# Kernel optimization log

Hardware: AMD Instinct MI355X
Metric: run time of the kernel (lower is better)

## Reference

```python
import jax, jax.numpy as jnp
import numpy as np

B, S, F_ATT, R, A = 1024, 96, 2048, 512, 512  # batch, att_size, att_feat_size, rnn_size, att_hid_size

def setup_inputs() -> dict:
    key = jax.random.key(0)
    ks = jax.random.split(key, 16)
    def lin(k, out_d, in_d):
        s = 1.0 / np.sqrt(in_d)
        kw, kb = jax.random.split(k)
        return (jax.random.uniform(kw, (out_d, in_d), jnp.float32, -s, s),
                jax.random.uniform(kb, (out_d,), jnp.float32, -s, s))
    W_ae, b_ae = lin(ks[0], R, F_ATT)   # att_embed Linear
    W_c,  b_c  = lin(ks[1], A, R)       # ctx2att
    W_s,  b_s  = lin(ks[2], A, R)       # sentinel_embed
    W_h,  b_h  = lin(ks[3], A, R)       # ho_embed
    W_al, b_al = lin(ks[4], 1, A)       # alpha_net
    W_o,  b_o  = lin(ks[5], R, R)       # att2h
    return {
        'h': jax.random.normal(ks[6], (B, R), jnp.float32),
        'sentinel': jax.random.normal(ks[7], (B, R), jnp.float32),
        'att_feats': jax.random.normal(ks[8], (B, S, F_ATT), jnp.float32),
        'W_ae': W_ae, 'b_ae': b_ae, 'W_c': W_c, 'b_c': b_c,
        'W_s': W_s, 'b_s': b_s, 'W_h': W_h, 'b_h': b_h,
        'W_al': W_al, 'b_al': b_al, 'W_o': W_o, 'b_o': b_o,
    }

def reference(h, sentinel, att_feats, W_ae, b_ae, W_c, b_c, W_s, b_s,
              W_h, b_h, W_al, b_al, W_o, b_o):
    # att_embed: Linear(2048->512) + ReLU (dropout = identity in eval)
    att = jax.nn.relu(jnp.einsum('bsf,rf->bsr', att_feats, W_ae) + b_ae)  # [B,S,R]
    att_embd = jnp.einsum('bsr,ar->bsa', att, W_c) + b_c                   # [B,S,A]
    sent_e = sentinel @ W_s.T + b_s                                        # [B,A]
    h_e = h @ W_h.T + b_h                                                  # [B,A]
    # concat sentinel slot in front of attention features
    img_all = jnp.concatenate([sentinel[:, None, :], att], axis=1)         # [B,S+1,R]
    img_all_embed = jnp.concatenate([sent_e[:, None, :], att_embd], axis=1)  # [B,S+1,A]
    hA = jnp.tanh(img_all_embed + h_e[:, None, :])                         # [B,S+1,A]
    logits = jnp.einsum('bsa,a->bs', hA, W_al[0]) + b_al[0]                # [B,S+1]
    alpha = jax.nn.softmax(logits, axis=-1)
    cHat = jnp.einsum('bs,bsr->br', alpha, img_all)                        # [B,R]
    atten_out = cHat + h
    return jnp.tanh(atten_out @ W_o.T + b_o)                               # [B,R]
```

## Files before the change

### kernel.cpp

```cpp
#include <hip/hip_runtime.h>

#define M1 98304
#define RDIM 512
#define FDIM 2048
#define SDIM 96
#define BM 96
#define BK 64

typedef __attribute__((ext_vector_type(8))) __bf16 bf16x8;
typedef __attribute__((ext_vector_type(4))) float f32x4;
typedef __attribute__((ext_vector_type(2))) float f32x2;

#define WAITV6 asm volatile("s_waitcnt vmcnt(6)" ::: "memory")
#define WAITV3 asm volatile("s_waitcnt vmcnt(3)" ::: "memory")
#define WAITV0 asm volatile("s_waitcnt vmcnt(0)" ::: "memory")
#define WAITL0 asm volatile("s_waitcnt lgkmcnt(0)" ::: "memory")
#define SBAR   __builtin_amdgcn_s_barrier()
#define SCHED0 __builtin_amdgcn_sched_barrier(0)

__device__ __forceinline__ float bf2f(unsigned short u){
  union { unsigned int i; float f; } v; v.i = ((unsigned int)u) << 16; return v.f;
}
__device__ __forceinline__ unsigned short f2bf(float f){
  union { float f; unsigned int i; } v; v.f = f;
  unsigned int r = v.i + 0x7FFFu + ((v.i >> 16) & 1u);
  return (unsigned short)(r >> 16);
}
__device__ __forceinline__ unsigned short f2bfn(float f){
  __bf16 b = (__bf16)f;
  return __builtin_bit_cast(unsigned short, b);
}
__device__ __forceinline__ float fast_tanh(float x){
  float e = __expf(2.f * x);
  return 1.f - 2.f / (e + 1.f);
}
__device__ __forceinline__ void gld_lds16(const void* g, void* l){
  __builtin_amdgcn_global_load_lds((const __attribute__((address_space(1))) void*)g,
                                   (__attribute__((address_space(3))) void*)l, 16, 0, 0);
}
__device__ __forceinline__ f32x4 mfma16(bf16x8 a, bf16x8 b, f32x4 c){
  return __builtin_amdgcn_mfma_f32_16x16x32_bf16(a, b, c, 0, 0, 0);
}
__device__ __forceinline__ f32x2 ntload2(const float* p){
  return __builtin_nontemporal_load(reinterpret_cast<const f32x2*>(p));
}

__device__ __forceinline__ void cat_store_a(const float* __restrict__ src,
                                            unsigned short* __restrict__ dst, int idx){
  float x = src[idx];
  int r = idx >> 9, c = idx & 511;
  unsigned short hi = f2bf(x);
  unsigned short lo = f2bf(x - bf2f(hi));
  unsigned short* p = dst + (long)r * 1536 + c;
  p[0] = hi; p[512] = lo; p[1024] = hi;
}
__device__ __forceinline__ void cat_store_w(const float* __restrict__ src,
                                            unsigned short* __restrict__ dst, int idx){
  float x = src[idx];
  int r = idx >> 9, c = idx & 511;
  unsigned short hi = f2bf(x);
  unsigned short lo = f2bf(x - bf2f(hi));
  unsigned short* p = dst + (long)r * 1536 + c;
  p[0] = hi; p[512] = hi; p[1024] = lo;
}

__global__ void k_convert(const float* W_ae, const float* W_c, const float* W_s,
                          const float* W_h, const float* W_o,
                          const float* h, const float* sent,
                          unsigned short* W_ae_bf, unsigned short* W_c_bf,
                          unsigned short* W_s_cat, unsigned short* W_h_cat,
                          unsigned short* W_o_cat, unsigned short* h_cat,
                          unsigned short* s_cat){
  const int stride = 1024 * 256;
  int i0 = blockIdx.x * 256 + threadIdx.x;
  switch (blockIdx.y) {
    case 0: for (int i = i0; i < 512*2048; i += stride) W_ae_bf[i] = f2bf(W_ae[i]); break;
    case 1: for (int i = i0; i < 512*512;  i += stride) W_c_bf[i]  = f2bf(W_c[i]);  break;
    case 2: for (int i = i0; i < 512*512;  i += stride) cat_store_w(W_s, W_s_cat, i); break;
    case 3: for (int i = i0; i < 512*512;  i += stride) cat_store_w(W_h, W_h_cat, i); break;
    case 4: for (int i = i0; i < 512*512;  i += stride) cat_store_w(W_o, W_o_cat, i); break;
    case 5: for (int i = i0; i < 1024*512; i += stride) cat_store_a(h, h_cat, i); break;
    case 6: for (int i = i0; i < 1024*512; i += stride) cat_store_a(sent, s_cat, i); break;
  }
}

__global__ __launch_bounds__(1024, 4) void k_fused(
    const float* __restrict__ Af, const unsigned short* __restrict__ Wae,
    const float* __restrict__ b_ae,
    const unsigned short* __restrict__ Wcg, const float* __restrict__ b_c,
    const float* __restrict__ h_e, const float* __restrict__ W_al,
    const float* __restrict__ sent_e, const float* __restrict__ sent,
    const float* __restrict__ hvec, unsigned short* __restrict__ atten_cat){
  __shared__ __align__(16) char smem[155648];
  unsigned short* As   = (unsigned short*)smem;
  unsigned short* Bs   = (unsigned short*)(smem + 24576);
  unsigned short* attL = (unsigned short*)smem;
  unsigned short* Wcs  = (unsigned short*)(smem + 98304);
  float* part = (float*)(smem + 131072);
  float* lg   = (float*)(smem + 131072 + 3072);
  float* alp  = (float*)(smem + 131072 + 3072 + 512);
  float* ssum = (float*)(smem + 131072 + 3072 + 1024);

  const int tid = threadIdx.x;
  const int w = tid >> 6, l = tid & 63;
  const int wm = w >> 3, wn = w & 7;
  const int b = blockIdx.x;
  const long m0 = (long)b * BM;
  const int g = l >> 4, r15 = l & 15;
  const int rs = r15 & 7;

  f32x4 acc[3][4];
#pragma unroll
  for (int i = 0; i < 3; ++i)
#pragma unroll
    for (int j = 0; j < 4; ++j) acc[i][j] = f32x4{0.f,0.f,0.f,0.f};

  {
    const int bswz = (l & 7) ^ (l >> 3);
    const unsigned short* bbase = Wae + (long)(w*32 + (l >> 3)) * FDIM + bswz*8;
    int aswz[3];
    const float* abase[3];
#pragma unroll
    for (int s = 0; s < 3; ++s) {
      int c = tid + s*1024;
      int row = c >> 5, kp = c & 31;
      abase[s] = Af + (m0 + row)*FDIM + kp*2;
      aswz[s] = row*BK + (((kp>>1) ^ ((row&7)<<1))<<2) + ((kp&1)<<1);
    }
    const int NT = FDIM / BK;
    f32x2 d0,d1,d2, e0,e1,e2;
    f32x2 f0 = {0,0}, f1 = {0,0}, f2 = {0,0};

    {
      f32x2 c0 = ntload2(abase[0]);
      f32x2 c1 = ntload2(abase[1]);
      f32x2 c2 = ntload2(abase[2]);
      SCHED0;
#pragma unroll
      for (int q = 0; q < 4; ++q)
        gld_lds16(bbase + (long)q*8*FDIM, Bs + w*2048 + q*512);
      SCHED0;
      d0 = ntload2(abase[0] + BK);
      d1 = ntload2(abase[1] + BK);
      d2 = ntload2(abase[2] + BK);
      e0 = ntload2(abase[0] + 2*BK);
      e1 = ntload2(abase[1] + 2*BK);
      e2 = ntload2(abase[2] + 2*BK);
      SCHED0;
      *reinterpret_cast<unsigned int*>(&As[aswz[0]]) =
          (unsigned int)f2bfn(c0.x) | ((unsigned int)f2bfn(c0.y) << 16);
      *reinterpret_cast<unsigned int*>(&As[aswz[1]]) =
          (unsigned int)f2bfn(c1.x) | ((unsigned int)f2bfn(c1.y) << 16);
      *reinterpret_cast<unsigned int*>(&As[aswz[2]]) =
          (unsigned int)f2bfn(c2.x) | ((unsigned int)f2bfn(c2.y) << 16);
      WAITV6; WAITL0; SCHED0; SBAR; SCHED0;
    }

    int cb = 0;
    for (int kt = 0; kt < NT; ++kt) {
      const int nb = cb ^ 1;
      if (kt + 1 < NT) {
        const long kof = (long)(kt+1) * BK;
#pragma unroll
        for (int q = 0; q < 4; ++q)
          gld_lds16(bbase + (long)q*8*FDIM + kof, Bs + nb*32768 + w*2048 + q*512);
      }
      SCHED0;
      if (kt + 3 < NT) {
        const long kof = (long)(kt+3) * BK;
        f0 = ntload2(abase[0] + kof);
        f1 = ntload2(abase[1] + kof);
        f2 = ntload2(abase[2] + kof);
      }
      SCHED0;
#pragma unroll
      for (int hh = 0; hh < 2; ++hh) {
        const int ko = ((g + 4*hh) ^ rs) << 3;
        bf16x8 afr[3], bfr[4];
#pragma unroll
        for (int i = 0; i < 3; ++i)
          afr[i] = *reinterpret_cast<const bf16x8*>(&As[cb*6144 + (wm*48 + i*16 + r15)*BK + ko]);
#pragma unroll
        for (int j = 0; j < 4; ++j)
          bfr[j] = *reinterpret_cast<const bf16x8*>(&Bs[cb*32768 + (wn*64 + j*16 + r15)*BK + ko]);
        __builtin_amdgcn_s_setprio(1);
#pragma unroll
        for (int i = 0; i < 3; ++i)
#pragma unroll
          for (int j = 0; j < 4; ++j)
            acc[i][j] = mfma16(afr[i], bfr[j], acc[i][j]);
        __builtin_amdgcn_s_setprio(0);
      }
      if (kt + 1 < NT) {
        *reinterpret_cast<unsigned int*>(&As[nb*6144 + aswz[0]]) =
            (unsigned int)f2bfn(d0.x) | ((unsigned int)f2bfn(d0.y) << 16);
        *reinterpret_cast<unsigned int*>(&As[nb*6144 + aswz[1]]) =
            (unsigned int)f2bfn(d1.x) | ((unsigned int)f2bfn(d1.y) << 16);
        *reinterpret_cast<unsigned int*>(&As[nb*6144 + aswz[2]]) =
            (unsigned int)f2bfn(d2.x) | ((unsigned int)f2bfn(d2.y) << 16);
        d0=e0; d1=e1; d2=e2; e0=f0; e1=f1; e2=f2;
        if (kt + 3 < NT) { WAITV3; } else { WAITV0; }
        WAITL0; SCHED0; SBAR; SCHED0;
        cb = nb;
      }
    }
  }
  __syncthreads();
  {
    float bb[4];
#pragma unroll
    for (int j = 0; j < 4; ++j) bb[j] = b_ae[wn*64 + j*16 + r15];
#pragma unroll
    for (int i = 0; i < 3; ++i)
#pragma unroll
      for (int r = 0; r < 4; ++r) {
        int row = wm*48 + i*16 + g*4 + r;
        int rs8 = row & 7;
#pragma unroll
        for (int j = 0; j < 4; ++j) {
          int col = wn*64 + j*16 + r15;
          float x = acc[i][j][r] + bb[j];
          x = x > 0.f ? x : 0.f;
          attL[row*512 + (((col>>3) ^ rs8)<<3) + (col&7)] = f2bfn(x);
        }
      }
  }
  __syncthreads();

#pragma unroll
  for (int i = 0; i < 3; ++i)
#pragma unroll
    for (int j = 0; j < 4; ++j) acc[i][j] = f32x4{0.f,0.f,0.f,0.f};
  {
    const int lr = l >> 2;
    const int bsl2 = (l & 3) ^ ((l >> 3) & 3);
    const int rs2 = (r15 >> 1) & 3;
    uint4 rr0, rr1;
    rr0 = *reinterpret_cast<const uint4*>(Wcg + (long)(w*32 + 0*16 + lr)*RDIM + bsl2*8);
    rr1 = *reinterpret_cast<const uint4*>(Wcg + (long)(w*32 + 1*16 + lr)*RDIM + bsl2*8);
    for (int kt = 0; kt < 16; ++kt) {
      *reinterpret_cast<uint4*>(&Wcs[w*1024 + 0*512 + l*8]) = rr0;
      *reinterpret_cast<uint4*>(&Wcs[w*1024 + 1*512 + l*8]) = rr1;
      if (kt < 15) {
        const int k0 = (kt+1)*32;
        rr0 = *reinterpret_cast<const uint4*>(Wcg + (long)(w*32 + 0*16 + lr)*RDIM + k0 + bsl2*8);
        rr1 = *reinterpret_cast<const uint4*>(Wcg + (long)(w*32 + 1*16 + lr)*RDIM + k0 + bsl2*8);
      }
      WAITL0; SCHED0; SBAR; SCHED0;
      bf16x8 afr[3], bfr[4];
#pragma unroll
      for (int i = 0; i < 3; ++i) {
        int ra = wm*48 + i*16 + r15;
        int grp = (kt<<2) + g;
        afr[i] = *reinterpret_cast<const bf16x8*>(&attL[ra*512 + ((grp ^ rs)<<3)]);
      }
#pragma unroll
      for (int j = 0; j < 4; ++j)
        bfr[j] = *reinterpret_cast<const bf16x8*>(&Wcs[(wn*64 + j*16 + r15)*32 + ((g ^ rs2)<<3)]);
      __builtin_amdgcn_s_setprio(1);
#pragma unroll
      for (int i = 0; i < 3; ++i)
#pragma unroll
        for (int j = 0; j < 4; ++j)
          acc[i][j] = mfma16(afr[i], bfr[j], acc[i][j]);
      __builtin_amdgcn_s_setprio(0);
      WAITL0; SCHED0; SBAR; SCHED0;
    }
  }
  {
    const float* hrow = h_e + (long)b * RDIM;
    float bb2[4], wa[4], he[4];
#pragma unroll
    for (int j = 0; j < 4; ++j) {
      int n = wn*64 + j*16 + r15;
      bb2[j] = b_c[n]; wa[j] = W_al[n]; he[j] = hrow[n];
    }
#pragma unroll
    for (int i = 0; i < 3; ++i)
#pragma unroll
      for (int r = 0; r < 4; ++r) {
        int lrow = wm*48 + i*16 + g*4 + r;
        float s = 0.f;
#pragma unroll
        for (int j = 0; j < 4; ++j) {
          float x = acc[i][j][r] + bb2[j] + he[j];
          s += fast_tanh(x) * wa[j];
        }
        s += __shfl_xor(s, 1); s += __shfl_xor(s, 2);
        s += __shfl_xor(s, 4); s += __shfl_xor(s, 8);
        if (r15 == 0) part[lrow*8 + wn] = s;
      }
  }
  __syncthreads();
  if (tid < 96) {
    float s = 0.f;
#pragma unroll
    for (int q = 0; q < 8; ++q) s += part[tid*8 + q];
    lg[1+tid] = s;
  }
  if (tid < 64) {
    float s = 0.f;
    for (int a = tid; a < 512; a += 64)
      s += fast_tanh(sent_e[(long)b*512 + a] + h_e[(long)b*512 + a]) * W_al[a];
    s += __shfl_xor(s, 1); s += __shfl_xor(s, 2); s += __shfl_xor(s, 4);
    s += __shfl_xor(s, 8); s += __shfl_xor(s, 16); s += __shfl_xor(s, 32);
    if (tid == 0) lg[0] = s;
  }
  __syncthreads();
  if (tid < 64) {
    float m = -1e30f;
    for (int i = tid; i < 97; i += 64) m = fmaxf(m, lg[i]);
#pragma unroll
    for (int k = 1; k < 64; k <<= 1) m = fmaxf(m, __shfl_xor(m, k));
    float ss = 0.f;
    for (int i = tid; i < 97; i += 64) { float e = __expf(lg[i] - m); alp[i] = e; ss += e; }
#pragma unroll
    for (int k = 1; k < 64; k <<= 1) ss += __shfl_xor(ss, k);
    if (tid == 0) ssum[0] = ss;
  }
  __syncthreads();
  if (tid < 97) alp[tid] *= (1.f / ssum[0]);
  __syncthreads();
  if (tid < 512) {
    const int col = tid;
    const int cg = col >> 3, ch = col & 7;
    float accv = alp[0] * sent[(long)b*512 + col];
#pragma unroll 4
    for (int s = 0; s < SDIM; ++s)
      accv += alp[s+1] * bf2f(attL[s*512 + ((cg ^ (s&7))<<3) + ch]);
    float x = accv + hvec[(long)b*512 + col];
    unsigned short hi = f2bf(x);
    unsigned short lo = f2bf(x - bf2f(hi));
    unsigned short* pp = atten_cat + (long)b*1536 + col;
    pp[0] = hi; pp[512] = lo; pp[1024] = hi;
  }
}

__device__ __forceinline__ void small_gemm_body(
    const unsigned short* __restrict__ Abf, const unsigned short* __restrict__ Wb,
    const float* __restrict__ bias, float* __restrict__ Cout, int do_tanh, int bx,
    unsigned short* As, unsigned short* Bs){
  const int tid = threadIdx.x;
  const int w = tid >> 6, l = tid & 63;
  const int wm = w >> 1, wn = w & 1;
  const int m0 = (bx >> 3) * 64, n0 = (bx & 7) * 64;
  const int K = 1536;
  f32x4 acc[2][2];
#pragma unroll
  for (int i = 0; i < 2; ++i)
#pragma unroll
    for (int j = 0; j < 2; ++j) acc[i][j] = f32x4{0.f,0.f,0.f,0.f};

  const int crow = l >> 2;
  const int bsl = (l & 3) ^ ((l >> 3) & 3);
  const unsigned short* arow_p = Abf + (long)(m0 + w*16 + crow)*K + bsl*8;
  const unsigned short* brow_p = Wb  + (long)(n0 + w*16 + crow)*K + bsl*8;

  gld_lds16(arow_p, As + w*512);
  gld_lds16(brow_p, Bs + w*512);
  __syncthreads();
  int cb = 0;
  for (int kt = 0; kt < 48; ++kt) {
    const int nb = cb ^ 1;
    if (kt + 1 < 48) {
      const int k0 = (kt+1) * 32;
      gld_lds16(arow_p + k0, As + nb*2048 + w*512);
      gld_lds16(brow_p + k0, Bs + nb*2048 + w*512);
    }
    bf16x8 afr[2], bfr[2];
    const int g = l >> 4, r15 = l & 15;
    const int rs2 = (r15 >> 1) & 3;
#pragma unroll
    for (int i = 0; i < 2; ++i)
      afr[i] = *reinterpret_cast<const bf16x8*>(As + cb*2048 + (wm*32 + i*16 + r15)*32 + ((g ^ rs2)*8));
#pragma unroll
    for (int j = 0; j < 2; ++j)
      bfr[j] = *reinterpret_cast<const bf16x8*>(Bs + cb*2048 + (wn*32 + j*16 + r15)*32 + ((g ^ rs2)*8));
#pragma unroll
    for (int i = 0; i < 2; ++i)
#pragma unroll
      for (int j = 0; j < 2; ++j)
        acc[i][j] = mfma16(afr[i], bfr[j], acc[i][j]);
    if (kt + 1 < 48) { __syncthreads(); cb = nb; }
  }
  const int r15 = l & 15, g = l >> 4;
#pragma unroll
  for (int i = 0; i < 2; ++i)
#pragma unroll
    for (int r = 0; r < 4; ++r) {
      int m = m0 + wm*32 + i*16 + g*4 + r;
#pragma unroll
      for (int j = 0; j < 2; ++j) {
        int n = n0 + wn*32 + j*16 + r15;
        float x = acc[i][j][r] + bias[n];
        if (do_tanh) x = fast_tanh(x);
        Cout[(long)m * 512 + n] = x;
      }
    }
}

__global__ __launch_bounds__(256) void k_gemm_small(
    const unsigned short* __restrict__ Abf, const unsigned short* __restrict__ Wb,
    const float* __restrict__ bias, float* __restrict__ Cout, int do_tanh){
  __shared__ __align__(16) unsigned short As[2*64*32];
  __shared__ __align__(16) unsigned short Bs[2*64*32];
  small_gemm_body(Abf, Wb, bias, Cout, do_tanh, blockIdx.x, As, Bs);
}

__global__ __launch_bounds__(256) void k_embed2(
    const unsigned short* __restrict__ h_cat, const unsigned short* __restrict__ W_h_cat,
    const float* __restrict__ b_h, float* __restrict__ h_e,
    const unsigned short* __restrict__ s_cat, const unsigned short* __restrict__ W_s_cat,
    const float* __restrict__ b_s, float* __restrict__ sent_e){
  __shared__ __align__(16) unsigned short As[2*64*32];
  __shared__ __align__(16) unsigned short Bs[2*64*32];
  if (blockIdx.y == 0) small_gemm_body(h_cat, W_h_cat, b_h, h_e, 0, blockIdx.x, As, Bs);
  else                 small_gemm_body(s_cat, W_s_cat, b_s, sent_e, 0, blockIdx.x, As, Bs);
}

extern "C" void kernel_launch(void* const* d_in, const int* in_sizes, int n_in,
                              void* d_out, int out_size, void* d_ws, size_t ws_size,
                              hipStream_t stream){
  (void)in_sizes; (void)n_in; (void)out_size; (void)ws_size;
  const float* h    = (const float*)d_in[0];
  const float* sent = (const float*)d_in[1];
  const float* feats= (const float*)d_in[2];
  const float* W_ae = (const float*)d_in[3];
  const float* b_ae = (const float*)d_in[4];
  const float* W_c  = (const float*)d_in[5];
  const float* b_c  = (const float*)d_in[6];
  const float* W_s  = (const float*)d_in[7];
  const float* b_s  = (const float*)d_in[8];
  const float* W_h  = (const float*)d_in[9];
  const float* b_h  = (const float*)d_in[10];
  const float* W_al = (const float*)d_in[11];
  const float* W_o  = (const float*)d_in[13];
  const float* b_o  = (const float*)d_in[14];
  float* out = (float*)d_out;

  char* p = (char*)d_ws;
  unsigned short* W_ae_bf = (unsigned short*)p; p += (size_t)512*2048*2;
  unsigned short* W_c_bf  = (unsigned short*)p; p += (size_t)512*512*2;
  unsigned short* W_s_cat = (unsigned short*)p; p += (size_t)512*1536*2;
  unsigned short* W_h_cat = (unsigned short*)p; p += (size_t)512*1536*2;
  unsigned short* W_o_cat = (unsigned short*)p; p += (size_t)512*1536*2;
  unsigned short* h_cat   = (unsigned short*)p; p += (size_t)1024*1536*2;
  unsigned short* s_cat   = (unsigned short*)p; p += (size_t)1024*1536*2;
  unsigned short* at_cat  = (unsigned short*)p; p += (size_t)1024*1536*2;
  float* h_e    = (float*)p; p += (size_t)1024*512*4;
  float* sent_e = (float*)p; p += (size_t)1024*512*4;

  k_convert<<<dim3(1024,7), 256, 0, stream>>>(W_ae, W_c, W_s, W_h, W_o, h, sent,
        W_ae_bf, W_c_bf, W_s_cat, W_h_cat, W_o_cat, h_cat, s_cat);
  k_embed2<<<dim3(128,2), 256, 0, stream>>>(h_cat, W_h_cat, b_h, h_e,
                                            s_cat, W_s_cat, b_s, sent_e);
  k_fused<<<1024, 1024, 0, stream>>>(feats, W_ae_bf, b_ae, W_c_bf, b_c,
                                     h_e, W_al, sent_e, sent, h, at_cat);
  k_gemm_small<<<128, 256, 0, stream>>>(at_cat, W_o_cat, b_o, out, 1);
}
```

Baseline: 397.5 us.

## Double-buffer W_c tiles via direct global-to-LDS loads and widen small-GEMM K tile

In the fused kernel, the second GEMM's W_c tiles now use a double-buffered LDS ring filled by direct global-to-LDS loads instead of register staging. That removes the register round trip and one barrier per k-step, and the softmax scratch buffers are moved to make room. In the small GEMMs the K tile doubles from 32 to 64 with a matching swizzle, halving loop iterations and barriers. The cost is more LDS per block, which may limit occupancy.

```diff
diff --git a/kernel.cpp b/kernel.cpp
--- a/kernel.cpp
+++ b/kernel.cpp
@@ -91,15 +91,15 @@
     const float* __restrict__ h_e, const float* __restrict__ W_al,
     const float* __restrict__ sent_e, const float* __restrict__ sent,
     const float* __restrict__ hvec, unsigned short* __restrict__ atten_cat){
-  __shared__ __align__(16) char smem[155648];
+  __shared__ __align__(16) char smem[163840];
   unsigned short* As   = (unsigned short*)smem;
   unsigned short* Bs   = (unsigned short*)(smem + 24576);
   unsigned short* attL = (unsigned short*)smem;
   unsigned short* Wcs  = (unsigned short*)(smem + 98304);
-  float* part = (float*)(smem + 131072);
-  float* lg   = (float*)(smem + 131072 + 3072);
-  float* alp  = (float*)(smem + 131072 + 3072 + 512);
-  float* ssum = (float*)(smem + 131072 + 3072 + 1024);
+  float* part = (float*)(smem + 98304);
+  float* lg   = (float*)(smem + 98304 + 3072);
+  float* alp  = (float*)(smem + 98304 + 3584);
+  float* ssum = (float*)(smem + 98304 + 4096);
 
   const int tid = threadIdx.x;
   const int w = tid >> 6, l = tid & 63;
@@ -235,18 +235,21 @@
     const int lr = l >> 2;
     const int bsl2 = (l & 3) ^ ((l >> 3) & 3);
     const int rs2 = (r15 >> 1) & 3;
-    uint4 rr0, rr1;
-    rr0 = *reinterpret_cast<const uint4*>(Wcg + (long)(w*32 + 0*16 + lr)*RDIM + bsl2*8);
-    rr1 = *reinterpret_cast<const uint4*>(Wcg + (long)(w*32 + 1*16 + lr)*RDIM + bsl2*8);
+#pragma unroll
+    for (int q = 0; q < 2; ++q)
+      gld_lds16(Wcg + (long)(w*32 + q*16 + lr)*RDIM + bsl2*8,
+                Wcs + w*1024 + q*512);
+    __syncthreads();
+    int cb = 0;
     for (int kt = 0; kt < 16; ++kt) {
-      *reinterpret_cast<uint4*>(&Wcs[w*1024 + 0*512 + l*8]) = rr0;
-      *reinterpret_cast<uint4*>(&Wcs[w*1024 + 1*512 + l*8]) = rr1;
-      if (kt < 15) {
+      const int nb = cb ^ 1;
+      if (kt + 1 < 16) {
         const int k0 = (kt+1)*32;
-        rr0 = *reinterpret_cast<const uint4*>(Wcg + (long)(w*32 + 0*16 + lr)*RDIM + k0 + bsl2*8);
-        rr1 = *reinterpret_cast<const uint4*>(Wcg + (long)(w*32 + 1*16 + lr)*RDIM + k0 + bsl2*8);
-      }
-      WAITL0; SCHED0; SBAR; SCHED0;
+#pragma unroll
+        for (int q = 0; q < 2; ++q)
+          gld_lds16(Wcg + (long)(w*32 + q*16 + lr)*RDIM + k0 + bsl2*8,
+                    Wcs + nb*16384 + w*1024 + q*512);
+      }
       bf16x8 afr[3], bfr[4];
 #pragma unroll
       for (int i = 0; i < 3; ++i) {
@@ -256,7 +259,7 @@
       }
 #pragma unroll
       for (int j = 0; j < 4; ++j)
-        bfr[j] = *reinterpret_cast<const bf16x8*>(&Wcs[(wn*64 + j*16 + r15)*32 + ((g ^ rs2)<<3)]);
+        bfr[j] = *reinterpret_cast<const bf16x8*>(&Wcs[cb*16384 + (wn*64 + j*16 + r15)*32 + ((g ^ rs2)<<3)]);
       __builtin_amdgcn_s_setprio(1);
 #pragma unroll
       for (int i = 0; i < 3; ++i)
@@ -264,7 +267,8 @@
         for (int j = 0; j < 4; ++j)
           acc[i][j] = mfma16(afr[i], bfr[j], acc[i][j]);
       __builtin_amdgcn_s_setprio(0);
-      WAITL0; SCHED0; SBAR; SCHED0;
+      __syncthreads();
+      cb = nb;
     }
   }
   {
@@ -345,45 +349,54 @@
   const int wm = w >> 1, wn = w & 1;
   const int m0 = (bx >> 3) * 64, n0 = (bx & 7) * 64;
   const int K = 1536;
+  const int g = l >> 4, r15 = l & 15;
+  const int rs = r15 & 7;
   f32x4 acc[2][2];
 #pragma unroll
   for (int i = 0; i < 2; ++i)
 #pragma unroll
     for (int j = 0; j < 2; ++j) acc[i][j] = f32x4{0.f,0.f,0.f,0.f};
 
-  const int crow = l >> 2;
-  const int bsl = (l & 3) ^ ((l >> 3) & 3);
-  const unsigned short* arow_p = Abf + (long)(m0 + w*16 + crow)*K + bsl*8;
-  const unsigned short* brow_p = Wb  + (long)(n0 + w*16 + crow)*K + bsl*8;
-
-  gld_lds16(arow_p, As + w*512);
-  gld_lds16(brow_p, Bs + w*512);
+  const int brow_in = l >> 3;
+  const int bswz = (l & 7) ^ brow_in;
+  const unsigned short* abase = Abf + (long)(m0 + w*16 + brow_in)*K + bswz*8;
+  const unsigned short* bbase = Wb  + (long)(n0 + w*16 + brow_in)*K + bswz*8;
+
+#pragma unroll
+  for (int q = 0; q < 2; ++q) {
+    gld_lds16(abase + (long)q*8*K, As + (w*16 + q*8)*64);
+    gld_lds16(bbase + (long)q*8*K, Bs + (w*16 + q*8)*64);
+  }
   __syncthreads();
   int cb = 0;
-  for (int kt = 0; kt < 48; ++kt) {
+  for (int kt = 0; kt < 24; ++kt) {
     const int nb = cb ^ 1;
-    if (kt + 1 < 48) {
-      const int k0 = (kt+1) * 32;
-      gld_lds16(arow_p + k0, As + nb*2048 + w*512);
-      gld_lds16(brow_p + k0, Bs + nb*2048 + w*512);
-    }
-    bf16x8 afr[2], bfr[2];
-    const int g = l >> 4, r15 = l & 15;
-    const int rs2 = (r15 >> 1) & 3;
-#pragma unroll
-    for (int i = 0; i < 2; ++i)
-      afr[i] = *reinterpret_cast<const bf16x8*>(As + cb*2048 + (wm*32 + i*16 + r15)*32 + ((g ^ rs2)*8));
-#pragma unroll
-    for (int j = 0; j < 2; ++j)
-      bfr[j] = *reinterpret_cast<const bf16x8*>(Bs + cb*2048 + (wn*32 + j*16 + r15)*32 + ((g ^ rs2)*8));
-#pragma unroll
-    for (int i = 0; i < 2; ++i)
+    if (kt + 1 < 24) {
+      const int k0 = (kt+1) * 64;
+#pragma unroll
+      for (int q = 0; q < 2; ++q) {
+        gld_lds16(abase + (long)q*8*K + k0, As + nb*4096 + (w*16 + q*8)*64);
+        gld_lds16(bbase + (long)q*8*K + k0, Bs + nb*4096 + (w*16 + q*8)*64);
+      }
+    }
+#pragma unroll
+    for (int h = 0; h < 2; ++h) {
+      const int ko = ((g + 4*h) ^ rs) << 3;
+      bf16x8 afr[2], bfr[2];
+#pragma unroll
+      for (int i = 0; i < 2; ++i)
+        afr[i] = *reinterpret_cast<const bf16x8*>(As + cb*4096 + (wm*32 + i*16 + r15)*64 + ko);
 #pragma unroll
       for (int j = 0; j < 2; ++j)
-        acc[i][j] = mfma16(afr[i], bfr[j], acc[i][j]);
-    if (kt + 1 < 48) { __syncthreads(); cb = nb; }
-  }
-  const int r15 = l & 15, g = l >> 4;
+        bfr[j] = *reinterpret_cast<const bf16x8*>(Bs + cb*4096 + (wn*32 + j*16 + r15)*64 + ko);
+#pragma unroll
+      for (int i = 0; i < 2; ++i)
+#pragma unroll
+        for (int j = 0; j < 2; ++j)
+          acc[i][j] = mfma16(afr[i], bfr[j], acc[i][j]);
+    }
+    if (kt + 1 < 24) { __syncthreads(); cb = nb; }
+  }
 #pragma unroll
   for (int i = 0; i < 2; ++i)
 #pragma unroll
@@ -402,8 +415,8 @@
 __global__ __launch_bounds__(256) void k_gemm_small(
     const unsigned short* __restrict__ Abf, const unsigned short* __restrict__ Wb,
     const float* __restrict__ bias, float* __restrict__ Cout, int do_tanh){
-  __shared__ __align__(16) unsigned short As[2*64*32];
-  __shared__ __align__(16) unsigned short Bs[2*64*32];
+  __shared__ __align__(16) unsigned short As[2*64*64];
+  __shared__ __align__(16) unsigned short Bs[2*64*64];
   small_gemm_body(Abf, Wb, bias, Cout, do_tanh, blockIdx.x, As, Bs);
 }
 
@@ -412,8 +425,8 @@
     const float* __restrict__ b_h, float* __restrict__ h_e,
     const unsigned short* __restrict__ s_cat, const unsigned short* __restrict__ W_s_cat,
     const float* __restrict__ b_s, float* __restrict__ sent_e){
-  __shared__ __align__(16) unsigned short As[2*64*32];
-  __shared__ __align__(16) unsigned short Bs[2*64*32];
+  __shared__ __align__(16) unsigned short As[2*64*64];
+  __shared__ __align__(16) unsigned short Bs[2*64*64];
   if (blockIdx.y == 0) small_gemm_body(h_cat, W_h_cat, b_h, h_e, 0, blockIdx.x, As, Bs);
   else                 small_gemm_body(s_cat, W_s_cat, b_s, sent_e, 0, blockIdx.x, As, Bs);
 }
```

Result: no change. 390.5 us (-1.8%).
